# Kernel optimization log

Hardware: AMD Instinct MI355X
Metric: run time of the kernel (lower is better)

## Reference

```python
import jax, jax.numpy as jnp
import numpy as np

# Module config (matches init_kwargs)
N_HEADS = 32        # query heads
MAX_SEQLEN = 2048
LOCAL_BLOCKS = 16
VERT_STRIDE = 8
BLOCK_SIZE = 64
HEAD_SIZE = 128
KV_HEADS = 8
BATCH = 2
SEQLEN = 1024       # per-sample length (equal-length varlen batch)


def _dense_sparse_mask(maxlen):
    """Local + strided block-sparse causal mask, heterogeneous heads.
    Returns bool [N_HEADS, maxlen, maxlen]; True = attend."""
    nb = MAX_SEQLEN // BLOCK_SIZE
    q_pos = jnp.arange(nb)[:, None]
    k_pos = jnp.arange(nb)[None, :]
    h = jnp.arange(N_HEADS)[:, None]
    # head-dependent vertical stride (homo_head=False)
    vert = ((jnp.arange(nb)[None, :] + h + 1) % VERT_STRIDE == 0)  # [H, nb]
    blk = (q_pos >= k_pos) & (((q_pos - k_pos) < LOCAL_BLOCKS)[None] | vert[:, None, :])  # [H, nb, nb]
    tok = jnp.repeat(jnp.repeat(blk, BLOCK_SIZE, axis=1), BLOCK_SIZE, axis=2)  # [H, S, S]
    causal = jnp.tril(jnp.ones((MAX_SEQLEN, MAX_SEQLEN), dtype=bool))
    tok = tok & causal[None]
    return tok[:, :maxlen, :maxlen]


def setup_inputs() -> dict:
    key = jax.random.key(0)
    kq, kk, kv = jax.random.split(key, 3)
    total = BATCH * SEQLEN
    q = jax.random.normal(kq, (total, N_HEADS, HEAD_SIZE), dtype=jnp.float32)
    k = jax.random.normal(kk, (total, KV_HEADS, HEAD_SIZE), dtype=jnp.float32)
    v = jax.random.normal(kv, (total, KV_HEADS, HEAD_SIZE), dtype=jnp.float32)
    cu_seqlens_k = jnp.arange(BATCH + 1, dtype=jnp.int32) * SEQLEN  # [0, 1024, 2048]
    return {"q": q, "k": k, "v": v, "cu_seqlens_k": cu_seqlens_k}


def reference(q, k, v, cu_seqlens_k):
    B = cu_seqlens_k.shape[0] - 1
    T, Hq, D = q.shape
    Hk = k.shape[1]
    r = Hq // Hk                      # q/kv head ratio (GQA)
    L = T // B                        # equal-length sequences
    scale = 1.0 / np.sqrt(D)

    mask = _dense_sparse_mask(L)      # [Hq, L, L]
    bias = jnp.where(mask, jnp.float32(0.0), jnp.finfo(jnp.float32).min)
    bias = bias.reshape(Hk, r, L, L)

    qb = q.reshape(B, L, Hk, r, D)
    kb = k.reshape(B, L, Hk, D)
    vb = v.reshape(B, L, Hk, D)

    scores = jnp.einsum('bqgrd,bkgd->bgrqk', qb, kb) * scale  # [B, Hk, r, L, L]
    attn = jax.nn.softmax(scores + bias[None], axis=-1)
    out = jnp.einsum('bgrqk,bkgd->bqgrd', attn, vb)           # [B, L, Hk, r, D]
    return out.reshape(T, Hq, D)
```

## Files before the change

### kernel.cpp

```cpp
#include <hip/hip_runtime.h>

typedef __attribute__((ext_vector_type(8))) short s8bf;
typedef __attribute__((ext_vector_type(4))) float f4;
typedef __attribute__((ext_vector_type(2))) unsigned u2;
typedef __attribute__((ext_vector_type(4))) unsigned u4;

#define HQ 32
#define HK 8
#define DH 128

static __device__ __forceinline__ unsigned cvtpk(float a, float b) {
  unsigned r;
  asm("v_cvt_pk_bf16_f32 %0, %1, %2" : "=v"(r) : "v"(a), "v"(b));
  return r;
}
union frag_u { s8bf v; unsigned u[4]; };

static __device__ __forceinline__ void gload_lds16(const short* g, short* l) {
  __builtin_amdgcn_global_load_lds(
      (const __attribute__((address_space(1))) void*)g,
      (__attribute__((address_space(3))) void*)l, 16, 0, 0);
}

#define WAIT_VM(N)                                         \
  do {                                                     \
    asm volatile("s_waitcnt vmcnt(" #N ")" ::: "memory");  \
    __builtin_amdgcn_sched_barrier(0);                     \
  } while (0)


__global__ void prep_kernel(const float* __restrict__ kg, const float* __restrict__ vg,
                            short* __restrict__ kbt, short* __restrict__ vbt) {
  const int blk = blockIdx.x;
  if (blk < 512) {
    const int gid = blk * 256 + threadIdx.x;
#pragma unroll
    for (int i = 0; i < 2; ++i) {
      int c = gid + i * 131072;
      int l16 = c & 15, quad = (c >> 4) & 3;
      int f = (c >> 6) & 15;
      int kt = (c >> 10) & 15;
      int bg = c >> 14;
      int b = bg >> 3, g = bg & 7;
      int key = kt * 64 + (f >> 2) * 16 + l16;
      int d0 = (f & 3) * 32 + quad * 8;
      const float* src = kg + (((size_t)(b * 1024 + key) * HK + g) * DH + d0);
      f4 a = *(const f4*)src, cc = *(const f4*)(src + 4);
      u4 w;
      w[0] = cvtpk(a[0], a[1]);   w[1] = cvtpk(a[2], a[3]);
      w[2] = cvtpk(cc[0], cc[1]); w[3] = cvtpk(cc[2], cc[3]);
      *(u4*)(kbt + (size_t)c * 8) = w;
    }
  } else {
    __shared__ short T[32 * 130];
    const int t = blk - 512;
    const int half = t & 1, tile = t >> 1;
    const int bg = tile >> 4, kt = tile & 15;
    const int b = bg >> 3, g = bg & 7;
#pragma unroll
    for (int i = 0; i < 4; ++i) {
      int e = threadIdx.x * 4 + i * 1024;
      int key = e >> 7, d = e & 127;
      f4 x = *(const f4*)(vg + (((size_t)(b * 1024 + kt * 64 + half * 32 + key) * HK + g) * DH + d));
      u2 w; w[0] = cvtpk(x[0], x[1]); w[1] = cvtpk(x[2], x[3]);
      *(u2*)&T[key * 130 + d] = w;
    }
    __syncthreads();
    short* dst = vbt + (size_t)(bg * 16 + kt) * 8192;
#pragma unroll
    for (int i = 0; i < 2; ++i) {
      int c = threadIdx.x + i * 256;
      int lane = c & 63, dt = c >> 6;
      int fidx = dt * 2 + half;
      int l16 = lane & 15, quad = (lane >> 4) & 3;
      int d = dt * 16 + l16;
      int k0 = quad * 4;
      int k1 = k0 + 16;
      u4 w;
      w[0] = (unsigned)(unsigned short)T[(k0 + 0) * 130 + d] |
             ((unsigned)(unsigned short)T[(k0 + 1) * 130 + d] << 16);
      w[1] = (unsigned)(unsigned short)T[(k0 + 2) * 130 + d] |
             ((unsigned)(unsigned short)T[(k0 + 3) * 130 + d] << 16);
      w[2] = (unsigned)(unsigned short)T[(k1 + 0) * 130 + d] |
             ((unsigned)(unsigned short)T[(k1 + 1) * 130 + d] << 16);
      w[3] = (unsigned)(unsigned short)T[(k1 + 2) * 130 + d] |
             ((unsigned)(unsigned short)T[(k1 + 3) * 130 + d] << 16);
      *(u4*)(dst + (size_t)(fidx * 64 + lane) * 8) = w;
    }
  }
}

__launch_bounds__(256, 2)
__global__ void fa_main(const float* __restrict__ qg, const short* __restrict__ kbt,
                        const short* __restrict__ vbt, float* __restrict__ out) {
  const int id  = blockIdx.x;
  const int g   = id & 7;
  const int s   = id >> 3;
  const int half = s >> 5, j = (s >> 3) & 3;
  const int t   = half ? j : 7 - j;
  const int rem = s & 7;
  const int b   = rem >> 2;
  const int h   = g * 4 + (rem & 3);
  const int bg  = b * 8 + g;
  const int qtA = 2 * t, qtB = 2 * t + 1;

  const int tid  = threadIdx.x;
  const int wave = tid >> 6, lane = tid & 63;
  const int l16  = lane & 15, quad = lane >> 4;
  const int qlocal = wave * 16 + l16;
  const int seq0 = b * 1024;

  __shared__ short smem[2][16384];

  const float qmul = 0.08838834764831845f * 1.4426950408889634f;
  const float* qpA = qg + ((size_t)(seq0 + qtA * 64 + qlocal) * HQ + h) * DH;
  const float* qpB = qg + ((size_t)(seq0 + qtB * 64 + qlocal) * HQ + h) * DH;
  s8bf qfA[4], qfB[4];
#pragma unroll
  for (int dk = 0; dk < 4; ++dk) {
    const float* pA = qpA + dk * 32 + quad * 8;
    const float* pB = qpB + dk * 32 + quad * 8;
    f4 a0 = *(const f4*)pA, a1 = *(const f4*)(pA + 4);
    f4 b0 = *(const f4*)pB, b1 = *(const f4*)(pB + 4);
    frag_u ta, tb;
    ta.u[0] = cvtpk(a0[0] * qmul, a0[1] * qmul);
    ta.u[1] = cvtpk(a0[2] * qmul, a0[3] * qmul);
    ta.u[2] = cvtpk(a1[0] * qmul, a1[1] * qmul);
    ta.u[3] = cvtpk(a1[2] * qmul, a1[3] * qmul);
    tb.u[0] = cvtpk(b0[0] * qmul, b0[1] * qmul);
    tb.u[1] = cvtpk(b0[2] * qmul, b0[3] * qmul);
    tb.u[2] = cvtpk(b1[0] * qmul, b1[1] * qmul);
    tb.u[3] = cvtpk(b1[2] * qmul, b1[3] * qmul);
    qfA[dk] = ta.v;
    qfB[dk] = tb.v;
  }

  float lA = 0.0f, lB = 0.0f;
  f4 oaccA[8], oaccB[8];
#pragma unroll
  for (int dt = 0; dt < 8; ++dt) { oaccA[dt] = (f4)(0.0f); oaccB[dt] = (f4)(0.0f); }

  const short* ktile = kbt + (size_t)bg * 16 * 8192;
  const short* vtile = vbt + (size_t)bg * 16 * 8192;

  __builtin_amdgcn_sched_barrier(0);

#pragma unroll
  for (int i = 0; i < 4; ++i) {
    int f = wave * 4 + i;
    gload_lds16(ktile + (size_t)(f * 64 + lane) * 8, &smem[0][f * 512]);
    gload_lds16(vtile + (size_t)(f * 64 + lane) * 8, &smem[0][8192 + f * 512]);
  }

  for (int kt = 0; kt <= qtB; ++kt) {
    const int cur = kt & 1;

    if (kt < qtB) {
      const short* kn = ktile + (size_t)(kt + 1) * 8192;
      const short* vn = vtile + (size_t)(kt + 1) * 8192;
      short* db = &smem[cur ^ 1][0];
#pragma unroll
      for (int i = 0; i < 4; ++i) {
        int f = wave * 4 + i;
        gload_lds16(kn + (size_t)(f * 64 + lane) * 8, db + f * 512);
        gload_lds16(vn + (size_t)(f * 64 + lane) * 8, db + 8192 + f * 512);
      }
      WAIT_VM(8);
    } else {
      WAIT_VM(0);
    }
    __builtin_amdgcn_s_barrier();
    __builtin_amdgcn_sched_barrier(0);

    const short* kb = &smem[cur][lane * 8];
    const short* vb = &smem[cur][8192 + lane * 8];

    f4 saccA[4], saccB[4];
#pragma unroll
    for (int ct = 0; ct < 4; ++ct) { saccA[ct] = (f4)(0.0f); saccB[ct] = (f4)(0.0f); }
    __builtin_amdgcn_s_setprio(1);
#pragma unroll
    for (int dk = 0; dk < 4; ++dk)
#pragma unroll
      for (int ct = 0; ct < 4; ++ct) {
        s8bf kf = *(const s8bf*)&kb[(ct * 4 + dk) * 512];
        saccA[ct] = __builtin_amdgcn_mfma_f32_16x16x32_bf16(kf, qfA[dk], saccA[ct], 0, 0, 0);
        saccB[ct] = __builtin_amdgcn_mfma_f32_16x16x32_bf16(kf, qfB[dk], saccB[ct], 0, 0, 0);
      }
    __builtin_amdgcn_s_setprio(0);

    if (kt >= qtA) {
      int thr = (kt == qtA) ? qlocal : -1;
#pragma unroll
      for (int ct = 0; ct < 4; ++ct)
#pragma unroll
        for (int i = 0; i < 4; ++i) {
          int key = ct * 16 + quad * 4 + i;
          if (key > thr) saccA[ct][i] = -1e30f;
        }
    }
    if (kt == qtB) {
#pragma unroll
      for (int ct = 0; ct < 4; ++ct)
#pragma unroll
        for (int i = 0; i < 4; ++i) {
          int key = ct * 16 + quad * 4 + i;
          if (key > qlocal) saccB[ct][i] = -1e30f;
        }
    }

    float rsA = 0.0f, rsB = 0.0f;
    unsigned pkA[4][2], pkB[4][2];
#pragma unroll
    for (int ct = 0; ct < 4; ++ct) {
      float a0 = exp2f(fminf(saccA[ct][0], 30.0f));
      float a1 = exp2f(fminf(saccA[ct][1], 30.0f));
      float a2 = exp2f(fminf(saccA[ct][2], 30.0f));
      float a3 = exp2f(fminf(saccA[ct][3], 30.0f));
      rsA += (a0 + a1) + (a2 + a3);
      pkA[ct][0] = cvtpk(a0, a1);
      pkA[ct][1] = cvtpk(a2, a3);
      float b0 = exp2f(fminf(saccB[ct][0], 30.0f));
      float b1 = exp2f(fminf(saccB[ct][1], 30.0f));
      float b2 = exp2f(fminf(saccB[ct][2], 30.0f));
      float b3 = exp2f(fminf(saccB[ct][3], 30.0f));
      rsB += (b0 + b1) + (b2 + b3);
      pkB[ct][0] = cvtpk(b0, b1);
      pkB[ct][1] = cvtpk(b2, b3);
    }
    lA += rsA;
    lB += rsB;

    __builtin_amdgcn_s_setprio(1);
#pragma unroll
    for (int ks = 0; ks < 2; ++ks) {
      frag_u frA, frB;
      frA.u[0] = pkA[2 * ks][0];
      frA.u[1] = pkA[2 * ks][1];
      frA.u[2] = pkA[2 * ks + 1][0];
      frA.u[3] = pkA[2 * ks + 1][1];
      frB.u[0] = pkB[2 * ks][0];
      frB.u[1] = pkB[2 * ks][1];
      frB.u[2] = pkB[2 * ks + 1][0];
      frB.u[3] = pkB[2 * ks + 1][1];
#pragma unroll
      for (int dt = 0; dt < 8; ++dt) {
        s8bf vf = *(const s8bf*)&vb[(dt * 2 + ks) * 512];
        oaccA[dt] = __builtin_amdgcn_mfma_f32_16x16x32_bf16(vf, frA.v, oaccA[dt], 0, 0, 0);
        oaccB[dt] = __builtin_amdgcn_mfma_f32_16x16x32_bf16(vf, frB.v, oaccB[dt], 0, 0, 0);
      }
    }
    __builtin_amdgcn_s_setprio(0);

    asm volatile("s_waitcnt lgkmcnt(0)" ::: "memory");
    __builtin_amdgcn_sched_barrier(0);
    __builtin_amdgcn_s_barrier();
  }

  float ltA = lA;
  ltA += __shfl_xor(ltA, 16);
  ltA += __shfl_xor(ltA, 32);
  float invA = 1.0f / ltA;
  float ltB = lB;
  ltB += __shfl_xor(ltB, 16);
  ltB += __shfl_xor(ltB, 32);
  float invB = 1.0f / ltB;

  float* opA = out + ((size_t)(seq0 + qtA * 64 + qlocal) * HQ + h) * DH;
  float* opB = out + ((size_t)(seq0 + qtB * 64 + qlocal) * HQ + h) * DH;
#pragma unroll
  for (int dt = 0; dt < 8; ++dt) {
    f4 wa, wb;
    wa[0] = oaccA[dt][0] * invA; wa[1] = oaccA[dt][1] * invA;
    wa[2] = oaccA[dt][2] * invA; wa[3] = oaccA[dt][3] * invA;
    wb[0] = oaccB[dt][0] * invB; wb[1] = oaccB[dt][1] * invB;
    wb[2] = oaccB[dt][2] * invB; wb[3] = oaccB[dt][3] * invB;
    *(f4*)(opA + dt * 16 + quad * 4) = wa;
    *(f4*)(opB + dt * 16 + quad * 4) = wb;
  }
}

extern "C" void kernel_launch(void* const* d_in, const int* in_sizes, int n_in,
                              void* d_out, int out_size, void* d_ws, size_t ws_size,
                              hipStream_t stream) {
  const float* q = (const float*)d_in[0];
  const float* k = (const float*)d_in[1];
  const float* v = (const float*)d_in[2];
  float* out = (float*)d_out;

  short* kbt = (short*)d_ws;
  short* vbt = kbt + (size_t)16 * 16 * 8192;

  prep_kernel<<<dim3(1024), 256, 0, stream>>>(k, v, kbt, vbt);
  fa_main<<<dim3(512), 256, 0, stream>>>(q, kbt, vbt, out);
}
```

Baseline: 127.2 us.

## Halve KV tile to 32 keys, skip masked A work, raise occupancy

The key/value tile shrinks from 64 to 32 keys, halving shared memory per block. This lets launch bounds request 4 blocks per SIMD instead of 2. Query tile A now skips its QK, softmax and PV MFMAs on the final 32-key steps, which lie entirely above its causal diagonal, cutting wasted masked compute. The block-to-tile scheduling also drops the heavy/light interleaved ordering for a plain linear order. The cost is twice as many loop iterations and barriers per block, plus possible register pressure from the higher occupancy target.

New measurement: 220.9 us. 73.7% more time.

```diff
diff --git a/kernel.cpp b/kernel.cpp
--- a/kernel.cpp
+++ b/kernel.cpp
@@ -90,19 +90,20 @@
   }
 }
 
-__launch_bounds__(256, 2)
+__launch_bounds__(256, 4)
 __global__ void fa_main(const float* __restrict__ qg, const short* __restrict__ kbt,
                         const short* __restrict__ vbt, float* __restrict__ out) {
   const int id  = blockIdx.x;
   const int g   = id & 7;
   const int s   = id >> 3;
-  const int half = s >> 5, j = (s >> 3) & 3;
-  const int t   = half ? j : 7 - j;
+  const int pt  = s >> 3;
   const int rem = s & 7;
   const int b   = rem >> 2;
   const int h   = g * 4 + (rem & 3);
   const int bg  = b * 8 + g;
-  const int qtA = 2 * t, qtB = 2 * t + 1;
+  const int qtA = 2 * pt, qtB = 2 * pt + 1;
+  const int kAmax = 4 * pt + 1;
+  const int kBmax = 4 * pt + 3;
 
   const int tid  = threadIdx.x;
   const int wave = tid >> 6, lane = tid & 63;
@@ -110,7 +111,7 @@
   const int qlocal = wave * 16 + l16;
   const int seq0 = b * 1024;
 
-  __shared__ short smem[2][16384];
+  __shared__ short smem[2][8192];
 
   const float qmul = 0.08838834764831845f * 1.4426950408889634f;
   const float* qpA = qg + ((size_t)(seq0 + qtA * 64 + qlocal) * HQ + h) * DH;
@@ -145,27 +146,31 @@
 
   __builtin_amdgcn_sched_barrier(0);
 
-#pragma unroll
-  for (int i = 0; i < 4; ++i) {
-    int f = wave * 4 + i;
-    gload_lds16(ktile + (size_t)(f * 64 + lane) * 8, &smem[0][f * 512]);
-    gload_lds16(vtile + (size_t)(f * 64 + lane) * 8, &smem[0][8192 + f * 512]);
-  }
-
-  for (int kt = 0; kt <= qtB; ++kt) {
+#define STAGE_TILE(J, BUF)                                                             \
+  do {                                                                                 \
+    const short* kb32 = ktile + (size_t)((J) >> 1) * 8192 + ((J) & 1) * 4096;          \
+    const short* vb32 = vtile + (size_t)((J) >> 1) * 8192 + ((J) & 1) * 512;           \
+    _Pragma("unroll")                                                                  \
+    for (int i = 0; i < 4; ++i) {                                                      \
+      int fidx = wave * 4 + i;                                                         \
+      if (fidx < 8) {                                                                  \
+        gload_lds16(kb32 + (size_t)(fidx * 64 + lane) * 8, &smem[BUF][fidx * 512]);    \
+      } else {                                                                         \
+        gload_lds16(vb32 + (size_t)((fidx - 8) * 128 + lane) * 8,                      \
+                    &smem[BUF][4096 + (fidx - 8) * 512]);                              \
+      }                                                                                \
+    }                                                                                  \
+  } while (0)
+
+  STAGE_TILE(0, 0);
+
+  for (int kt = 0; kt <= kBmax; ++kt) {
     const int cur = kt & 1;
-
-    if (kt < qtB) {
-      const short* kn = ktile + (size_t)(kt + 1) * 8192;
-      const short* vn = vtile + (size_t)(kt + 1) * 8192;
-      short* db = &smem[cur ^ 1][0];
-#pragma unroll
-      for (int i = 0; i < 4; ++i) {
-        int f = wave * 4 + i;
-        gload_lds16(kn + (size_t)(f * 64 + lane) * 8, db + f * 512);
-        gload_lds16(vn + (size_t)(f * 64 + lane) * 8, db + 8192 + f * 512);
-      }
-      WAIT_VM(8);
+    const bool aAct = (kt <= kAmax);
+
+    if (kt < kBmax) {
+      STAGE_TILE(kt + 1, cur ^ 1);
+      WAIT_VM(4);
     } else {
       WAIT_VM(0);
     }
@@ -173,82 +178,81 @@
     __builtin_amdgcn_sched_barrier(0);
 
     const short* kb = &smem[cur][lane * 8];
-    const short* vb = &smem[cur][8192 + lane * 8];
-
-    f4 saccA[4], saccB[4];
-#pragma unroll
-    for (int ct = 0; ct < 4; ++ct) { saccA[ct] = (f4)(0.0f); saccB[ct] = (f4)(0.0f); }
+    const short* vb = &smem[cur][4096 + lane * 8];
+
+    f4 saccA[2], saccB[2];
+#pragma unroll
+    for (int ct = 0; ct < 2; ++ct) { saccA[ct] = (f4)(0.0f); saccB[ct] = (f4)(0.0f); }
     __builtin_amdgcn_s_setprio(1);
 #pragma unroll
     for (int dk = 0; dk < 4; ++dk)
 #pragma unroll
-      for (int ct = 0; ct < 4; ++ct) {
+      for (int ct = 0; ct < 2; ++ct) {
         s8bf kf = *(const s8bf*)&kb[(ct * 4 + dk) * 512];
-        saccA[ct] = __builtin_amdgcn_mfma_f32_16x16x32_bf16(kf, qfA[dk], saccA[ct], 0, 0, 0);
+        if (aAct)
+          saccA[ct] = __builtin_amdgcn_mfma_f32_16x16x32_bf16(kf, qfA[dk], saccA[ct], 0, 0, 0);
         saccB[ct] = __builtin_amdgcn_mfma_f32_16x16x32_bf16(kf, qfB[dk], saccB[ct], 0, 0, 0);
       }
     __builtin_amdgcn_s_setprio(0);
 
-    if (kt >= qtA) {
-      int thr = (kt == qtA) ? qlocal : -1;
-#pragma unroll
-      for (int ct = 0; ct < 4; ++ct)
+    if (aAct && kt >= 4 * pt) {
+      int thrA = qlocal - (kt - 4 * pt) * 32;
+#pragma unroll
+      for (int ct = 0; ct < 2; ++ct)
 #pragma unroll
         for (int i = 0; i < 4; ++i) {
           int key = ct * 16 + quad * 4 + i;
-          if (key > thr) saccA[ct][i] = -1e30f;
+          if (key > thrA) saccA[ct][i] = -1e30f;
         }
     }
-    if (kt == qtB) {
-#pragma unroll
-      for (int ct = 0; ct < 4; ++ct)
+    if (kt >= 4 * pt + 2) {
+      int thrB = qlocal - (kt - 4 * pt - 2) * 32;
+#pragma unroll
+      for (int ct = 0; ct < 2; ++ct)
 #pragma unroll
         for (int i = 0; i < 4; ++i) {
           int key = ct * 16 + quad * 4 + i;
-          if (key > qlocal) saccB[ct][i] = -1e30f;
+          if (key > thrB) saccB[ct][i] = -1e30f;
         }
     }
 
-    float rsA = 0.0f, rsB = 0.0f;
-    unsigned pkA[4][2], pkB[4][2];
-#pragma unroll
-    for (int ct = 0; ct < 4; ++ct) {
-      float a0 = exp2f(fminf(saccA[ct][0], 30.0f));
-      float a1 = exp2f(fminf(saccA[ct][1], 30.0f));
-      float a2 = exp2f(fminf(saccA[ct][2], 30.0f));
-      float a3 = exp2f(fminf(saccA[ct][3], 30.0f));
-      rsA += (a0 + a1) + (a2 + a3);
-      pkA[ct][0] = cvtpk(a0, a1);
-      pkA[ct][1] = cvtpk(a2, a3);
-      float b0 = exp2f(fminf(saccB[ct][0], 30.0f));
-      float b1 = exp2f(fminf(saccB[ct][1], 30.0f));
-      float b2 = exp2f(fminf(saccB[ct][2], 30.0f));
-      float b3 = exp2f(fminf(saccB[ct][3], 30.0f));
-      rsB += (b0 + b1) + (b2 + b3);
-      pkB[ct][0] = cvtpk(b0, b1);
-      pkB[ct][1] = cvtpk(b2, b3);
-    }
-    lA += rsA;
-    lB += rsB;
+    frag_u frA, frB;
+    if (aAct) {
+      float rsA = 0.0f;
+#pragma unroll
+      for (int ct = 0; ct < 2; ++ct) {
+        float a0 = exp2f(fminf(saccA[ct][0], 30.0f));
+        float a1 = exp2f(fminf(saccA[ct][1], 30.0f));
+        float a2 = exp2f(fminf(saccA[ct][2], 30.0f));
+        float a3 = exp2f(fminf(saccA[ct][3], 30.0f));
+        rsA += (a0 + a1) + (a2 + a3);
+        frA.u[ct * 2 + 0] = cvtpk(a0, a1);
+        frA.u[ct * 2 + 1] = cvtpk(a2, a3);
+      }
+      lA += rsA;
+    }
+    {
+      float rsB = 0.0f;
+#pragma unroll
+      for (int ct = 0; ct < 2; ++ct) {
+        float b0 = exp2f(fminf(saccB[ct][0], 30.0f));
+        float b1 = exp2f(fminf(saccB[ct][1], 30.0f));
+        float b2 = exp2f(fminf(saccB[ct][2], 30.0f));
+        float b3 = exp2f(fminf(saccB[ct][3], 30.0f));
+        rsB += (b0 + b1) + (b2 + b3);
+        frB.u[ct * 2 + 0] = cvtpk(b0, b1);
+        frB.u[ct * 2 + 1] = cvtpk(b2, b3);
+      }
+      lB += rsB;
+    }
 
     __builtin_amdgcn_s_setprio(1);
 #pragma unroll
-    for (int ks = 0; ks < 2; ++ks) {
-      frag_u frA, frB;
-      frA.u[0] = pkA[2 * ks][0];
-      frA.u[1] = pkA[2 * ks][1];
-      frA.u[2] = pkA[2 * ks + 1][0];
-      frA.u[3] = pkA[2 * ks + 1][1];
-      frB.u[0] = pkB[2 * ks][0];
-      frB.u[1] = pkB[2 * ks][1];
-      frB.u[2] = pkB[2 * ks + 1][0];
-      frB.u[3] = pkB[2 * ks + 1][1];
-#pragma unroll
-      for (int dt = 0; dt < 8; ++dt) {
-        s8bf vf = *(const s8bf*)&vb[(dt * 2 + ks) * 512];
+    for (int dt = 0; dt < 8; ++dt) {
+      s8bf vf = *(const s8bf*)&vb[dt * 512];
+      if (aAct)
         oaccA[dt] = __builtin_amdgcn_mfma_f32_16x16x32_bf16(vf, frA.v, oaccA[dt], 0, 0, 0);
-        oaccB[dt] = __builtin_amdgcn_mfma_f32_16x16x32_bf16(vf, frB.v, oaccB[dt], 0, 0, 0);
-      }
+      oaccB[dt] = __builtin_amdgcn_mfma_f32_16x16x32_bf16(vf, frB.v, oaccB[dt], 0, 0, 0);
     }
     __builtin_amdgcn_s_setprio(0);
 
```
